# Kernel optimization log

Hardware: AMD Instinct MI355X
Metric: run time of the kernel (lower is better)

Reference implementation:

```python
import jax, jax.numpy as jnp
import numpy as np

NQ = 12          # qubits per node circuit
DIM = 2 ** NQ    # statevector length 4096


def _apply_1q(state, U, w):
    """Apply 2x2 gate U (shared (2,2) or per-batch (B,2,2)) on wire w. state: (B, 4096)."""
    B = state.shape[0]
    l, r = 2 ** w, 2 ** (NQ - w - 1)
    s = state.reshape(B, l, 2, r)
    if U.ndim == 2:
        s = jnp.einsum('ij,bajc->baic', U, s)
    else:
        s = jnp.einsum('bij,bajc->baic', U, s)
    return s.reshape(B, DIM)


_G = np.zeros((2, 2, 2, 2), np.complex64)  # CNOT tensor: (c_out, t_out, c_in, t_in)
for _c in range(2):
    for _t in range(2):
        _G[_c, _t ^ _c, _c, _t] = 1.0


def _apply_cnot(state, c, t):
    B = state.shape[0]
    lo, hi = min(c, t), max(c, t)
    a, m, r = 2 ** lo, 2 ** (hi - lo - 1), 2 ** (NQ - hi - 1)
    s = state.reshape(B, a, 2, m, 2, r)
    T = _G if c == lo else _G.transpose(1, 0, 3, 2)  # reorder to (lo, hi) axis convention
    s = jnp.einsum('ijkl,bakcld->baicjd', jnp.asarray(T), s)
    return s.reshape(B, DIM)


def _ry_mats(ang):
    """Per-node RY matrices. ang: (B,) -> (B,2,2) complex64."""
    c, s = jnp.cos(ang / 2), jnp.sin(ang / 2)
    U = jnp.stack([jnp.stack([c, -s], -1), jnp.stack([s, c], -1)], -2)
    return U.astype(jnp.complex64)


def _rot_mat(p):
    """PennyLane Rot(phi, theta, omega) = RZ(omega) RY(theta) RZ(phi)."""
    phi, th, om = p[0], p[1], p[2]
    c, s = jnp.cos(th / 2), jnp.sin(th / 2)
    U = jnp.stack([
        jnp.stack([jnp.exp(-0.5j * (phi + om)) * c, -jnp.exp(0.5j * (phi - om)) * s]),
        jnp.stack([jnp.exp(-0.5j * (phi - om)) * s, jnp.exp(0.5j * (phi + om)) * c]),
    ])
    return U.astype(jnp.complex64)


# (rot_wire_a, rot_wire_b, (cnot_control, cnot_target)) blocks of the TTN circuit
_BLOCKS = [(0, 1, (0, 1)), (2, 3, (3, 2)), (4, 5, (4, 5)), (6, 7, (7, 6)),
           (8, 9, (8, 9)), (10, 11, (11, 10)), (1, 2, (1, 2)), (5, 6, (6, 5)),
           (9, 10, (10, 9)), (2, 5, (2, 5)), (5, 9, (5, 9))]


def _ttn_circuit(M, theta):
    """Batched 12-qubit TTN circuit. M: (B,12) angles, theta: (69,). Returns <Z_9>: (B,)."""
    B = M.shape[0]
    state = jnp.zeros((B, DIM), jnp.complex64).at[:, 0].set(1.0)
    for w in range(NQ):
        state = _apply_1q(state, _ry_mats(M[:, w]), w)
    k = 0
    for w1, w2, (c, t) in _BLOCKS:
        state = _apply_1q(state, _rot_mat(theta[3 * k:3 * k + 3]), w1); k += 1
        state = _apply_1q(state, _rot_mat(theta[3 * k:3 * k + 3]), w2); k += 1
        state = _apply_cnot(state, c, t)
    state = _apply_1q(state, _rot_mat(theta[3 * k:3 * k + 3]), 4)  # final Rot, k = 22
    probs = (state.real ** 2 + state.imag ** 2).reshape(B, 2 ** 9, 2, 2 ** 2)
    return probs[:, :, 0].sum((1, 2)) - probs[:, :, 1].sum((1, 2))  # <Z on wire 9>


def setup_inputs() -> dict:
    key = jax.random.key(0)
    kx, ke, ki, ko, kt = jax.random.split(key, 5)
    N, E, D = 1024, 8192, 4
    X = jax.random.normal(kx, (N, D), dtype=jnp.float32)
    e = jax.random.uniform(ke, (E,), dtype=jnp.float32)
    idx_i = jax.random.randint(ki, (E,), 0, N)
    idx_o = jax.random.randint(ko, (E,), 0, N)
    Ri = jnp.zeros((N, E), jnp.float32).at[idx_i, jnp.arange(E)].set(1.0)
    Ro = jnp.zeros((N, E), jnp.float32).at[idx_o, jnp.arange(E)].set(1.0)
    theta = jax.random.uniform(kt, (69,), dtype=jnp.float32, maxval=2 * np.pi)
    return {"X": X, "e": e, "Ri": Ri, "Ro": Ro, "theta": theta}


def reference(X, e, Ri, Ro, theta):
    bo = Ro.T @ X                     # [E, D] features of outgoing nodes
    bi = Ri.T @ X                     # [E, D]
    mi = (Ri * e) @ bo                # [N, D] edge-weighted aggregation
    mo = (Ro * e) @ bi                # [N, D]
    M = jnp.concatenate([mi, mo, X], axis=1)   # [N, 12] -> circuit angles
    z = _ttn_circuit(M, theta)
    return (jnp.pi * (1.0 - z)).astype(jnp.float32)  # 2*pi*(1 - <Z>)/2 per node
```

## Files before the change

### kernel.cpp

```cpp
#include <hip/hip_runtime.h>
#include <math.h>

#define NN 1024
#define NE 8192

struct c32 { float x, y; };
__device__ __forceinline__ c32 cmul(c32 a, c32 b)  { return {a.x*b.x - a.y*b.y, a.x*b.y + a.y*b.x}; }
__device__ __forceinline__ c32 cmulc(c32 a, c32 b) { return {a.x*b.x + a.y*b.y, a.y*b.x - a.x*b.y}; }
__device__ __forceinline__ c32 cadd(c32 a, c32 b)  { return {a.x + b.x, a.y + b.y}; }

__device__ __forceinline__ void rot2(const float* __restrict__ t3, c32 A[2][2]) {
  float phi = t3[0], th = t3[1], om = t3[2];
  float s, c;   sincosf(0.5f * th, &s, &c);
  float sa, ca; sincosf(0.5f * (phi + om), &sa, &ca);
  float sb, cb; sincosf(0.5f * (phi - om), &sb, &cb);
  A[0][0] = {  ca * c, -sa * c };
  A[0][1] = { -cb * s, -sb * s };
  A[1][0] = {  cb * s, -sb * s };
  A[1][1] = {  ca * c,  sa * c };
}

__global__ void k_extract(const float* __restrict__ Ri, const float* __restrict__ Ro,
                          int* __restrict__ idx_i, int* __restrict__ idx_o,
                          float* __restrict__ mimo) {
  const int per = NN * NE / 4;
  int tid    = blockIdx.x * blockDim.x + threadIdx.x;
  int stride = gridDim.x * blockDim.x;
  if (tid < (2 * NN * 4) / 4) ((float4*)mimo)[tid] = make_float4(0.f, 0.f, 0.f, 0.f);
  for (int t = tid; t < 2 * per; t += stride) {
    bool first = (t < per);
    const float4* src = first ? (const float4*)Ri : (const float4*)Ro;
    int* dst          = first ? idx_i : idx_o;
    int q = first ? t : t - per;
    float4 v = src[q];
    if (v.x != 0.f || v.y != 0.f || v.z != 0.f || v.w != 0.f) {
      int base = q * 4;
      int n = base >> 13;
      int k = base & (NE - 1);
      if (v.x != 0.f) dst[k + 0] = n;
      if (v.y != 0.f) dst[k + 1] = n;
      if (v.z != 0.f) dst[k + 2] = n;
      if (v.w != 0.f) dst[k + 3] = n;
    }
  }
}

__global__ void k_edges(const float* __restrict__ X, const float* __restrict__ e,
                        const int* __restrict__ idx_i, const int* __restrict__ idx_o,
                        float* __restrict__ mi, float* __restrict__ mo) {
  int k = blockIdx.x * blockDim.x + threadIdx.x;
  if (k >= NE) return;
  int ni = idx_i[k], no = idx_o[k];
  float w = e[k];
  float4 xo = ((const float4*)X)[no];
  float4 xi = ((const float4*)X)[ni];
  atomicAdd(&mi[ni * 4 + 0], w * xo.x);
  atomicAdd(&mi[ni * 4 + 1], w * xo.y);
  atomicAdd(&mi[ni * 4 + 2], w * xo.z);
  atomicAdd(&mi[ni * 4 + 3], w * xo.w);
  atomicAdd(&mo[no * 4 + 0], w * xi.x);
  atomicAdd(&mo[no * 4 + 1], w * xi.y);
  atomicAdd(&mo[no * 4 + 2], w * xi.z);
  atomicAdd(&mo[no * 4 + 3], w * xi.w);
}

__device__ __forceinline__ void gate1(float2* __restrict__ S, int tid, int pairs, int b,
                                      const c32 (*U)[2]) {
  c32 U00 = U[0][0], U01 = U[0][1], U10 = U[1][0], U11 = U[1][1];
  int mask = (1 << b) - 1;
  for (int t = tid; t < pairs; t += 64) {
    int i0 = ((t & ~mask) << 1) | (t & mask);
    int i1 = i0 | (1 << b);
    float2 av = S[i0], bv = S[i1];
    c32 a = {av.x, av.y}, c = {bv.x, bv.y};
    c32 r0 = cadd(cmul(U00, a), cmul(U01, c));
    c32 r1 = cadd(cmul(U10, a), cmul(U11, c));
    S[i0] = {r0.x, r0.y};
    S[i1] = {r1.x, r1.y};
  }
}

__device__ __forceinline__ void cnotg(float2* __restrict__ S, int tid, int quarter, int cb, int tb) {
  int lo = cb < tb ? cb : tb, hi = cb < tb ? tb : cb;
  int lmask = (1 << lo) - 1, hmask = (1 << hi) - 1;
  for (int t = tid; t < quarter; t += 64) {
    int x = ((t & ~lmask) << 1) | (t & lmask);
    x = ((x & ~hmask) << 1) | (x & hmask);
    int i0 = x | (1 << cb);
    int i1 = i0 | (1 << tb);
    float2 a = S[i0], b = S[i1];
    S[i0] = b; S[i1] = a;
  }
}

__global__ void __launch_bounds__(64) k_sv2(const float* __restrict__ X,
                                            const float* __restrict__ theta,
                                            const float* __restrict__ mi,
                                            const float* __restrict__ mo,
                                            float* __restrict__ out) {
  __shared__ float2 SA[256];
  __shared__ float2 SB[16];
  __shared__ c32 R[23][2][2];
  const int tid = threadIdx.x;
  const int n = blockIdx.x;

  if (tid < 23) {
    c32 A[2][2];
    rot2(theta + 3 * tid, A);
    R[tid][0][0] = A[0][0]; R[tid][0][1] = A[0][1];
    R[tid][1][0] = A[1][0]; R[tid][1][1] = A[1][1];
  }

  float4 miv = ((const float4*)mi)[n];
  float4 mov = ((const float4*)mo)[n];
  float4 xv  = ((const float4*)X)[n];
  float ang[12] = { miv.x, miv.y, miv.z, miv.w, mov.x, mov.y, mov.z, mov.w, xv.x, xv.y, xv.z, xv.w };
  float cw[12], sw[12];
  #pragma unroll
  for (int w = 0; w < 12; w++) sincosf(0.5f * ang[w], &sw[w], &cw[w]);

  #pragma unroll
  for (int j = 0; j < 4; j++) {
    int i = tid + 64 * j;
    float amp = 1.f;
    #pragma unroll
    for (int w = 0; w < 8; w++) amp *= ((i >> (7 - w)) & 1) ? sw[w] : cw[w];
    SA[i] = {amp, 0.f};
  }
  if (tid < 16) {
    float amp = 1.f;
    #pragma unroll
    for (int w = 8; w < 12; w++) amp *= ((tid >> (11 - w)) & 1) ? sw[w] : cw[w];
    SB[tid] = {amp, 0.f};
  }
  __syncthreads();

  gate1(SA, tid, 128, 7, R[0]);  __syncthreads();
  gate1(SA, tid, 128, 6, R[1]);  __syncthreads();
  cnotg(SA, tid, 64, 7, 6);      __syncthreads();
  gate1(SA, tid, 128, 5, R[2]);  __syncthreads();
  gate1(SA, tid, 128, 4, R[3]);  __syncthreads();
  cnotg(SA, tid, 64, 4, 5);      __syncthreads();
  gate1(SA, tid, 128, 3, R[4]);  __syncthreads();
  gate1(SA, tid, 128, 2, R[5]);  __syncthreads();
  cnotg(SA, tid, 64, 3, 2);      __syncthreads();
  gate1(SA, tid, 128, 1, R[6]);  __syncthreads();
  gate1(SA, tid, 128, 0, R[7]);  __syncthreads();
  cnotg(SA, tid, 64, 0, 1);      __syncthreads();
  gate1(SB, tid, 8, 3, R[8]);    __syncthreads();
  gate1(SB, tid, 8, 2, R[9]);    __syncthreads();
  cnotg(SB, tid, 4, 3, 2);       __syncthreads();
  gate1(SB, tid, 8, 1, R[10]);   __syncthreads();
  gate1(SB, tid, 8, 0, R[11]);   __syncthreads();
  cnotg(SB, tid, 4, 0, 1);       __syncthreads();
  gate1(SA, tid, 128, 6, R[12]); __syncthreads();
  gate1(SA, tid, 128, 5, R[13]); __syncthreads();
  cnotg(SA, tid, 64, 6, 5);      __syncthreads();
  gate1(SA, tid, 128, 2, R[14]); __syncthreads();
  gate1(SA, tid, 128, 1, R[15]); __syncthreads();
  cnotg(SA, tid, 64, 1, 2);      __syncthreads();
  gate1(SB, tid, 8, 2, R[16]);   __syncthreads();
  gate1(SB, tid, 8, 1, R[17]);   __syncthreads();
  cnotg(SB, tid, 4, 1, 2);       __syncthreads();
  gate1(SA, tid, 128, 5, R[18]); __syncthreads();
  gate1(SA, tid, 128, 2, R[19]); __syncthreads();
  cnotg(SA, tid, 64, 5, 2);      __syncthreads();
  gate1(SA, tid, 128, 3, R[22]); __syncthreads();

  float p00 = 0.f, p11 = 0.f; c32 p01 = {0.f, 0.f};
  #pragma unroll
  for (int m = 0; m < 2; m++) {
    int ao = tid + 64 * m;
    int i0 = ((ao & ~3) << 1) | (ao & 3);
    int i1 = i0 | 4;
    float2 a0 = SA[i0], a1 = SA[i1];
    p00 += a0.x * a0.x + a0.y * a0.y;
    p11 += a1.x * a1.x + a1.y * a1.y;
    p01 = cadd(p01, cmulc({a0.x, a0.y}, {a1.x, a1.y}));
  }
  #pragma unroll
  for (int m = 1; m < 64; m <<= 1) {
    p00 += __shfl_xor(p00, m, 64);
    p11 += __shfl_xor(p11, m, 64);
    p01.x += __shfl_xor(p01.x, m, 64);
    p01.y += __shfl_xor(p01.y, m, 64);
  }

  float q00 = 0.f, q11 = 0.f; c32 q01 = {0.f, 0.f};
  #pragma unroll
  for (int ao = 0; ao < 8; ao++) {
    int i0 = ((ao & ~3) << 1) | (ao & 3);
    int i1 = i0 | 4;
    float2 b0 = SB[i0], b1 = SB[i1];
    q00 += b0.x * b0.x + b0.y * b0.y;
    q11 += b1.x * b1.x + b1.y * b1.y;
    q01 = cadd(q01, cmulc({b0.x, b0.y}, {b1.x, b1.y}));
  }

  c32 U4[4][4];
  #pragma unroll
  for (int i = 0; i < 2; i++)
    #pragma unroll
    for (int p = 0; p < 2; p++)
      #pragma unroll
      for (int j = 0; j < 2; j++)
        #pragma unroll
        for (int q = 0; q < 2; q++)
          U4[2 * i + p][2 * j + q] = cmul(R[20][i][j], R[21][p][q]);
  #pragma unroll
  for (int c = 0; c < 4; c++) { c32 t = U4[2][c]; U4[2][c] = U4[3][c]; U4[3][c] = t; }

  c32 rho5[2][2] = { {{p00, 0.f}, p01}, {{p01.x, -p01.y}, {p11, 0.f}} };
  c32 rho9[2][2] = { {{q00, 0.f}, q01}, {{q01.x, -q01.y}, {q11, 0.f}} };
  float z = 0.f;
  #pragma unroll
  for (int a = 0; a < 4; a++)
    #pragma unroll
    for (int b = 0; b < 4; b++) {
      c32 m = {0.f, 0.f};
      #pragma unroll
      for (int i = 0; i < 4; i++) {
        c32 t = cmulc(U4[i][a], U4[i][b]);
        if (i & 1) { m.x -= t.x; m.y -= t.y; } else { m = cadd(m, t); }
      }
      c32 rr = cmul(rho5[a >> 1][b >> 1], rho9[a & 1][b & 1]);
      z += m.x * rr.x - m.y * rr.y;
    }

  if (tid == 0) out[n] = 3.14159265358979f * (1.f - z);
}

extern "C" void kernel_launch(void* const* d_in, const int* in_sizes, int n_in,
                              void* d_out, int out_size, void* d_ws, size_t ws_size,
                              hipStream_t stream) {
  (void)in_sizes; (void)n_in; (void)out_size; (void)ws_size;
  const float* X     = (const float*)d_in[0];
  const float* e     = (const float*)d_in[1];
  const float* Ri    = (const float*)d_in[2];
  const float* Ro    = (const float*)d_in[3];
  const float* theta = (const float*)d_in[4];
  float* out = (float*)d_out;

  char* ws = (char*)d_ws;
  int*   idx_i = (int*)(ws);
  int*   idx_o = (int*)(ws + 32768);
  float* mi    = (float*)(ws + 65536);
  float* mo    = (float*)(ws + 65536 + 16384);

  hipLaunchKernelGGL(k_extract, dim3(4096), dim3(256), 0, stream, Ri, Ro, idx_i, idx_o, mi);
  hipLaunchKernelGGL(k_edges,   dim3(NE / 256), dim3(256), 0, stream, X, e, idx_i, idx_o, mi, mo);
  hipLaunchKernelGGL(k_sv2,     dim3(NN), dim3(64), 0, stream, X, theta, mi, mo, out);
}
```

Measured before the change: 36.43 us.

## Keep statevector in registers and apply gates via wave shuffles

Replaces the shared-memory statevector simulation and its many barriers with a register-resident layout. The 256-amplitude subsystem is held as four amplitudes per lane, and gates act through cross-lane shuffles. The 16-amplitude subsystem is held entirely in each lane's registers. Fast-math __sincosf replaces sincosf. This removes LDS traffic and roughly thirty __syncthreads per node, at the cost of extra register pressure and lower-precision trig.

```diff
diff --git a/kernel.cpp b/kernel.cpp
--- a/kernel.cpp
+++ b/kernel.cpp
@@ -8,6 +8,9 @@
 __device__ __forceinline__ c32 cmul(c32 a, c32 b)  { return {a.x*b.x - a.y*b.y, a.x*b.y + a.y*b.x}; }
 __device__ __forceinline__ c32 cmulc(c32 a, c32 b) { return {a.x*b.x + a.y*b.y, a.y*b.x - a.x*b.y}; }
 __device__ __forceinline__ c32 cadd(c32 a, c32 b)  { return {a.x + b.x, a.y + b.y}; }
+
+__device__ __forceinline__ float sx(float v, int m)  { return __shfl_xor(v, m, 64); }
+__device__ __forceinline__ float sidx(float v, int l){ return __shfl(v, l, 64); }
 
 __device__ __forceinline__ void rot2(const float* __restrict__ t3, c32 A[2][2]) {
   float phi = t3[0], th = t3[1], om = t3[2];
@@ -64,51 +67,67 @@
   atomicAdd(&mo[no * 4 + 3], w * xi.w);
 }
 
-__device__ __forceinline__ void gate1(float2* __restrict__ S, int tid, int pairs, int b,
-                                      const c32 (*U)[2]) {
-  c32 U00 = U[0][0], U01 = U[0][1], U10 = U[1][0], U11 = U[1][1];
-  int mask = (1 << b) - 1;
-  for (int t = tid; t < pairs; t += 64) {
+__device__ __forceinline__ void rot_lane(c32* a, const c32 (*U)[2], int lane, int b) {
+  int s = (lane >> b) & 1;
+  c32 us = s ? U[1][1] : U[0][0];
+  c32 up = s ? U[1][0] : U[0][1];
+  #pragma unroll
+  for (int r = 0; r < 4; r++) {
+    c32 p = { sx(a[r].x, 1 << b), sx(a[r].y, 1 << b) };
+    a[r] = cadd(cmul(us, a[r]), cmul(up, p));
+  }
+}
+
+__device__ __forceinline__ void rot_pair(c32& x0, c32& x1, const c32 (*U)[2]) {
+  c32 n0 = cadd(cmul(U[0][0], x0), cmul(U[0][1], x1));
+  c32 n1 = cadd(cmul(U[1][0], x0), cmul(U[1][1], x1));
+  x0 = n0; x1 = n1;
+}
+
+__device__ __forceinline__ void cnot_ll(c32* a, int lane, int c, int t) {
+  int idx = lane ^ (((lane >> c) & 1) << t);
+  #pragma unroll
+  for (int r = 0; r < 4; r++) a[r] = { sidx(a[r].x, idx), sidx(a[r].y, idx) };
+}
+
+__device__ __forceinline__ void rotB(c32* bb, const c32 (*U)[2], int k) {
+  int mask = (1 << k) - 1;
+  #pragma unroll
+  for (int t = 0; t < 8; t++) {
     int i0 = ((t & ~mask) << 1) | (t & mask);
-    int i1 = i0 | (1 << b);
-    float2 av = S[i0], bv = S[i1];
-    c32 a = {av.x, av.y}, c = {bv.x, bv.y};
-    c32 r0 = cadd(cmul(U00, a), cmul(U01, c));
-    c32 r1 = cadd(cmul(U10, a), cmul(U11, c));
-    S[i0] = {r0.x, r0.y};
-    S[i1] = {r1.x, r1.y};
-  }
-}
-
-__device__ __forceinline__ void cnotg(float2* __restrict__ S, int tid, int quarter, int cb, int tb) {
-  int lo = cb < tb ? cb : tb, hi = cb < tb ? tb : cb;
-  int lmask = (1 << lo) - 1, hmask = (1 << hi) - 1;
-  for (int t = tid; t < quarter; t += 64) {
-    int x = ((t & ~lmask) << 1) | (t & lmask);
-    x = ((x & ~hmask) << 1) | (x & hmask);
-    int i0 = x | (1 << cb);
-    int i1 = i0 | (1 << tb);
-    float2 a = S[i0], b = S[i1];
-    S[i0] = b; S[i1] = a;
-  }
-}
-
-__global__ void __launch_bounds__(64) k_sv2(const float* __restrict__ X,
+    int i1 = i0 | (1 << k);
+    c32 b0 = bb[i0], b1 = bb[i1];
+    bb[i0] = cadd(cmul(U[0][0], b0), cmul(U[0][1], b1));
+    bb[i1] = cadd(cmul(U[1][0], b0), cmul(U[1][1], b1));
+  }
+}
+
+__device__ __forceinline__ void cnotB(c32* bb, int c, int t) {
+  int lo = c < t ? c : t, hi = c < t ? t : c;
+  int lm = (1 << lo) - 1, hm = (1 << hi) - 1;
+  #pragma unroll
+  for (int q = 0; q < 4; q++) {
+    int x = ((q & ~lm) << 1) | (q & lm);
+    x = ((x & ~hm) << 1) | (x & hm);
+    int i0 = x | (1 << c), i1 = i0 | (1 << t);
+    c32 tmp = bb[i0]; bb[i0] = bb[i1]; bb[i1] = tmp;
+  }
+}
+
+__global__ void __launch_bounds__(64) k_sv3(const float* __restrict__ X,
                                             const float* __restrict__ theta,
                                             const float* __restrict__ mi,
                                             const float* __restrict__ mo,
                                             float* __restrict__ out) {
-  __shared__ float2 SA[256];
-  __shared__ float2 SB[16];
   __shared__ c32 R[23][2][2];
-  const int tid = threadIdx.x;
+  const int lane = threadIdx.x;
   const int n = blockIdx.x;
 
-  if (tid < 23) {
+  if (lane < 23) {
     c32 A[2][2];
-    rot2(theta + 3 * tid, A);
-    R[tid][0][0] = A[0][0]; R[tid][0][1] = A[0][1];
-    R[tid][1][0] = A[1][0]; R[tid][1][1] = A[1][1];
+    rot2(theta + 3 * lane, A);
+    R[lane][0][0] = A[0][0]; R[lane][0][1] = A[0][1];
+    R[lane][1][0] = A[1][0]; R[lane][1][1] = A[1][1];
   }
 
   float4 miv = ((const float4*)mi)[n];
@@ -117,73 +136,72 @@
   float ang[12] = { miv.x, miv.y, miv.z, miv.w, mov.x, mov.y, mov.z, mov.w, xv.x, xv.y, xv.z, xv.w };
   float cw[12], sw[12];
   #pragma unroll
-  for (int w = 0; w < 12; w++) sincosf(0.5f * ang[w], &sw[w], &cw[w]);
-
-  #pragma unroll
-  for (int j = 0; j < 4; j++) {
-    int i = tid + 64 * j;
+  for (int w = 0; w < 12; w++) __sincosf(0.5f * ang[w], &sw[w], &cw[w]);
+
+  c32 a[4];
+  {
+    float lfac = 1.f;
+    #pragma unroll
+    for (int w = 2; w < 8; w++) lfac *= ((lane >> (7 - w)) & 1) ? sw[w] : cw[w];
+    a[0] = { cw[0] * cw[1] * lfac, 0.f };
+    a[1] = { cw[0] * sw[1] * lfac, 0.f };
+    a[2] = { sw[0] * cw[1] * lfac, 0.f };
+    a[3] = { sw[0] * sw[1] * lfac, 0.f };
+  }
+  c32 bb[16];
+  #pragma unroll
+  for (int i = 0; i < 16; i++) {
     float amp = 1.f;
     #pragma unroll
-    for (int w = 0; w < 8; w++) amp *= ((i >> (7 - w)) & 1) ? sw[w] : cw[w];
-    SA[i] = {amp, 0.f};
-  }
-  if (tid < 16) {
-    float amp = 1.f;
-    #pragma unroll
-    for (int w = 8; w < 12; w++) amp *= ((tid >> (11 - w)) & 1) ? sw[w] : cw[w];
-    SB[tid] = {amp, 0.f};
+    for (int w = 8; w < 12; w++) amp *= ((i >> (11 - w)) & 1) ? sw[w] : cw[w];
+    bb[i] = { amp, 0.f };
   }
   __syncthreads();
 
-  gate1(SA, tid, 128, 7, R[0]);  __syncthreads();
-  gate1(SA, tid, 128, 6, R[1]);  __syncthreads();
-  cnotg(SA, tid, 64, 7, 6);      __syncthreads();
-  gate1(SA, tid, 128, 5, R[2]);  __syncthreads();
-  gate1(SA, tid, 128, 4, R[3]);  __syncthreads();
-  cnotg(SA, tid, 64, 4, 5);      __syncthreads();
-  gate1(SA, tid, 128, 3, R[4]);  __syncthreads();
-  gate1(SA, tid, 128, 2, R[5]);  __syncthreads();
-  cnotg(SA, tid, 64, 3, 2);      __syncthreads();
-  gate1(SA, tid, 128, 1, R[6]);  __syncthreads();
-  gate1(SA, tid, 128, 0, R[7]);  __syncthreads();
-  cnotg(SA, tid, 64, 0, 1);      __syncthreads();
-  gate1(SB, tid, 8, 3, R[8]);    __syncthreads();
-  gate1(SB, tid, 8, 2, R[9]);    __syncthreads();
-  cnotg(SB, tid, 4, 3, 2);       __syncthreads();
-  gate1(SB, tid, 8, 1, R[10]);   __syncthreads();
-  gate1(SB, tid, 8, 0, R[11]);   __syncthreads();
-  cnotg(SB, tid, 4, 0, 1);       __syncthreads();
-  gate1(SA, tid, 128, 6, R[12]); __syncthreads();
-  gate1(SA, tid, 128, 5, R[13]); __syncthreads();
-  cnotg(SA, tid, 64, 6, 5);      __syncthreads();
-  gate1(SA, tid, 128, 2, R[14]); __syncthreads();
-  gate1(SA, tid, 128, 1, R[15]); __syncthreads();
-  cnotg(SA, tid, 64, 1, 2);      __syncthreads();
-  gate1(SB, tid, 8, 2, R[16]);   __syncthreads();
-  gate1(SB, tid, 8, 1, R[17]);   __syncthreads();
-  cnotg(SB, tid, 4, 1, 2);       __syncthreads();
-  gate1(SA, tid, 128, 5, R[18]); __syncthreads();
-  gate1(SA, tid, 128, 2, R[19]); __syncthreads();
-  cnotg(SA, tid, 64, 5, 2);      __syncthreads();
-  gate1(SA, tid, 128, 3, R[22]); __syncthreads();
-
+  rot_pair(a[0], a[2], R[0]);  rot_pair(a[1], a[3], R[0]);
+  rot_pair(a[0], a[1], R[1]);  rot_pair(a[2], a[3], R[1]);
+  { c32 t = a[2]; a[2] = a[3]; a[3] = t; }
+  rot_lane(a, R[2], lane, 5);
+  rot_lane(a, R[3], lane, 4);
+  cnot_ll(a, lane, 4, 5);
+  rot_lane(a, R[4], lane, 3);
+  rot_lane(a, R[5], lane, 2);
+  cnot_ll(a, lane, 3, 2);
+  rot_lane(a, R[6], lane, 1);
+  rot_lane(a, R[7], lane, 0);
+  cnot_ll(a, lane, 0, 1);
+  rot_pair(a[0], a[1], R[12]); rot_pair(a[2], a[3], R[12]);
+  rot_lane(a, R[13], lane, 5);
+  a[1] = { sx(a[1].x, 32), sx(a[1].y, 32) };
+  a[3] = { sx(a[3].x, 32), sx(a[3].y, 32) };
+  rot_lane(a, R[14], lane, 2);
+  rot_lane(a, R[15], lane, 1);
+  cnot_ll(a, lane, 1, 2);
+  rot_lane(a, R[18], lane, 5);
+  rot_lane(a, R[19], lane, 2);
+  cnot_ll(a, lane, 5, 2);
+  rot_lane(a, R[22], lane, 3);
+
+  rotB(bb, R[8], 3);  rotB(bb, R[9], 2);  cnotB(bb, 3, 2);
+  rotB(bb, R[10], 1); rotB(bb, R[11], 0); cnotB(bb, 0, 1);
+  rotB(bb, R[16], 2); rotB(bb, R[17], 1); cnotB(bb, 1, 2);
+
+  int s5 = (lane >> 2) & 1;
   float p00 = 0.f, p11 = 0.f; c32 p01 = {0.f, 0.f};
   #pragma unroll
-  for (int m = 0; m < 2; m++) {
-    int ao = tid + 64 * m;
-    int i0 = ((ao & ~3) << 1) | (ao & 3);
-    int i1 = i0 | 4;
-    float2 a0 = SA[i0], a1 = SA[i1];
-    p00 += a0.x * a0.x + a0.y * a0.y;
-    p11 += a1.x * a1.x + a1.y * a1.y;
-    p01 = cadd(p01, cmulc({a0.x, a0.y}, {a1.x, a1.y}));
+  for (int r = 0; r < 4; r++) {
+    c32 pr = { sx(a[r].x, 4), sx(a[r].y, 4) };
+    float nn = a[r].x * a[r].x + a[r].y * a[r].y;
+    c32 cp = cmulc(a[r], pr);
+    p00 += s5 ? 0.f : nn;
+    p11 += s5 ? nn : 0.f;
+    p01.x += s5 ? 0.f : cp.x;
+    p01.y += s5 ? 0.f : cp.y;
   }
   #pragma unroll
   for (int m = 1; m < 64; m <<= 1) {
-    p00 += __shfl_xor(p00, m, 64);
-    p11 += __shfl_xor(p11, m, 64);
-    p01.x += __shfl_xor(p01.x, m, 64);
-    p01.y += __shfl_xor(p01.y, m, 64);
+    p00 += sx(p00, m); p11 += sx(p11, m);
+    p01.x += sx(p01.x, m); p01.y += sx(p01.y, m);
   }
 
   float q00 = 0.f, q11 = 0.f; c32 q01 = {0.f, 0.f};
@@ -191,10 +209,10 @@
   for (int ao = 0; ao < 8; ao++) {
     int i0 = ((ao & ~3) << 1) | (ao & 3);
     int i1 = i0 | 4;
-    float2 b0 = SB[i0], b1 = SB[i1];
+    c32 b0 = bb[i0], b1 = bb[i1];
     q00 += b0.x * b0.x + b0.y * b0.y;
     q11 += b1.x * b1.x + b1.y * b1.y;
-    q01 = cadd(q01, cmulc({b0.x, b0.y}, {b1.x, b1.y}));
+    q01 = cadd(q01, cmulc(b0, b1));
   }
 
   c32 U4[4][4];
@@ -214,20 +232,20 @@
   c32 rho9[2][2] = { {{q00, 0.f}, q01}, {{q01.x, -q01.y}, {q11, 0.f}} };
   float z = 0.f;
   #pragma unroll
-  for (int a = 0; a < 4; a++)
-    #pragma unroll
-    for (int b = 0; b < 4; b++) {
+  for (int aa = 0; aa < 4; aa++)
+    #pragma unroll
+    for (int b2 = 0; b2 < 4; b2++) {
       c32 m = {0.f, 0.f};
       #pragma unroll
       for (int i = 0; i < 4; i++) {
-        c32 t = cmulc(U4[i][a], U4[i][b]);
+        c32 t = cmulc(U4[i][aa], U4[i][b2]);
         if (i & 1) { m.x -= t.x; m.y -= t.y; } else { m = cadd(m, t); }
       }
-      c32 rr = cmul(rho5[a >> 1][b >> 1], rho9[a & 1][b & 1]);
+      c32 rr = cmul(rho5[aa >> 1][b2 >> 1], rho9[aa & 1][b2 & 1]);
       z += m.x * rr.x - m.y * rr.y;
     }
 
-  if (tid == 0) out[n] = 3.14159265358979f * (1.f - z);
+  if (lane == 0) out[n] = 3.14159265358979f * (1.f - z);
 }
 
 extern "C" void kernel_launch(void* const* d_in, const int* in_sizes, int n_in,
@@ -249,5 +267,5 @@
 
   hipLaunchKernelGGL(k_extract, dim3(4096), dim3(256), 0, stream, Ri, Ro, idx_i, idx_o, mi);
   hipLaunchKernelGGL(k_edges,   dim3(NE / 256), dim3(256), 0, stream, X, e, idx_i, idx_o, mi, mo);
-  hipLaunchKernelGGL(k_sv2,     dim3(NN), dim3(64), 0, stream, X, theta, mi, mo, out);
-}
+  hipLaunchKernelGGL(k_sv3,     dim3(NN), dim3(64), 0, stream, X, theta, mi, mo, out);
+}
```

New measurement: 40.16 us. 1.1x slower.
